# Kernel tuning notes

Hardware: AMD Instinct MI355X
Metric: run time of the kernel (lower is better)

The kernel has to match this reference:

```python
import jax, jax.numpy as jnp
import numpy as np

B = 64; WIN_IN = 32; WIN_OUT = 8; NODES = 128; FEAT = 16
HID = 64; LSTM_H = 32; CLASSES = 10
N = B * WIN_IN * NODES      # 262144 total nodes in batched graph
E = 8 * N                   # 2097152 edges (avg degree 8)


def setup_inputs() -> dict:
    key = jax.random.key(0)
    ks = jax.random.split(key, 16)
    p = lambda k, s: (jax.random.normal(k, s, dtype=jnp.float32) * 0.05)
    return {
        "x": jax.random.normal(ks[0], (N, FEAT), dtype=jnp.float32),
        "edge_index": jax.random.randint(ks[1], (2, E), 0, N, dtype=jnp.int32),
        "W1": p(ks[2], (FEAT, HID)),   "b1": p(ks[3], (HID,)),
        "W2": p(ks[4], (HID, FEAT)),   "b2": p(ks[5], (FEAT,)),
        "Wih": p(ks[6], (4 * LSTM_H, NODES * FEAT)),
        "Whh": p(ks[7], (4 * LSTM_H, LSTM_H)),
        "bih": p(ks[8], (4 * LSTM_H,)), "bhh": p(ks[9], (4 * LSTM_H,)),
        "Wfc1": p(ks[10], (16, LSTM_H)), "bfc1": p(ks[11], (16,)),
        "Wfc2": p(ks[12], (CLASSES, 16)), "bfc2": p(ks[13], (CLASSES,)),
    }


def _gcn_conv(x, row, col, W, b):
    # PyG GCNConv: x' = D^-1/2 (A+I) D^-1/2 (x W) + b, deg counted at target (col)
    h = x @ W
    deg = jax.ops.segment_sum(jnp.ones(row.shape[0], jnp.float32), col, num_segments=N) + 1.0
    dinv = jax.lax.rsqrt(deg)
    msg = h[row] * (dinv[row] * dinv[col])[:, None]          # [E, F]
    agg = jax.ops.segment_sum(msg, col, num_segments=N)
    agg = agg + h * (dinv * dinv)[:, None]                   # self-loop term
    return agg + b


def _lstm(seq, Wih, Whh, bih, bhh):
    # seq: [B, T, D] -> outputs [B, T, H]; torch gate order i, f, g, o
    xs = jnp.transpose(seq, (1, 0, 2))
    h0 = jnp.zeros((seq.shape[0], LSTM_H), seq.dtype)
    bias = bih + bhh

    def step(carry, xt):
        h, c = carry
        g = xt @ Wih.T + h @ Whh.T + bias
        i, f, gg, o = jnp.split(g, 4, axis=-1)
        c = jax.nn.sigmoid(f) * c + jax.nn.sigmoid(i) * jnp.tanh(gg)
        h = jax.nn.sigmoid(o) * jnp.tanh(c)
        return (h, c), h

    _, hs = jax.lax.scan(step, (h0, h0), xs)
    return jnp.transpose(hs, (1, 0, 2))


def reference(x, edge_index, W1, b1, W2, b2, Wih, Whh, bih, bhh, Wfc1, bfc1, Wfc2, bfc2):
    row, col = edge_index[0], edge_index[1]
    h = jax.nn.relu(_gcn_conv(x, row, col, W1, b1))
    h = jax.nn.relu(_gcn_conv(h, row, col, W2, b2))
    h = h.reshape(B, WIN_IN, NODES * FEAT)
    h = _lstm(h, Wih, Whh, bih, bhh)
    h = h[:, -WIN_OUT:, :]
    h = jax.nn.relu(h @ Wfc1.T + bfc1)
    h = h @ Wfc2.T + bfc2
    return h.reshape(-1, CLASSES)
```

## Files before the change

kernel.cpp:

```cpp
#include <hip/hip_runtime.h>
#include <hip/hip_fp16.h>

#define NN      262144
#define EDGES   2097152
#define FEATD   16
#define HIDD    64
#define LSTMH   32
#define BATCH   64
#define WIN     32
#define WOUT    8
#define NCLS    10
#define ROWD    2048
#define KCHUNKS 16
#define KSPAN   (ROWD / KCHUNKS)

#define NB2     512
#define NW      512
#define CAPB    4608
#define NBLK    256
#define CHUNK   (EDGES / NBLK)

typedef __fp16 half4v __attribute__((ext_vector_type(4)));
typedef float  float4v __attribute__((ext_vector_type(4)));

__global__ void k_hist(const int* __restrict__ ei, int* __restrict__ hist2d) {
    __shared__ int h[NB2];
    int blk = blockIdx.x, tid = threadIdx.x;
    for (int l = tid; l < NB2; l += 256) h[l] = 0;
    __syncthreads();
    int e0 = blk * CHUNK;
    for (int i = tid; i < CHUNK; i += 256)
        atomicAdd(&h[ei[EDGES + e0 + i] >> 9], 1);
    __syncthreads();
    for (int l = tid; l < NB2; l += 256) hist2d[l * NBLK + blk] = h[l];
}

__global__ void k_scan2(int* __restrict__ hist2d, int* __restrict__ bcnt) {
    __shared__ int s[NBLK];
    int b = blockIdx.x, tid = threadIdx.x;
    int v = hist2d[b * NBLK + tid];
    s[tid] = v;
    __syncthreads();
    for (int off = 1; off < NBLK; off <<= 1) {
        int t = (tid >= off) ? s[tid - off] : 0;
        __syncthreads();
        s[tid] += t;
        __syncthreads();
    }
    hist2d[b * NBLK + tid] = s[tid] - v;
    if (tid == NBLK - 1) bcnt[b] = s[tid];
}

__global__ void k_place(const int* __restrict__ ei, const int* __restrict__ hist2d,
                        int* __restrict__ bdata) {
    __shared__ int curp[NB2];
    int blk = blockIdx.x, tid = threadIdx.x;
    for (int l = tid; l < NB2; l += 256) curp[l] = hist2d[l * NBLK + blk];
    __syncthreads();
    int e0 = blk * CHUNK;
    for (int i = tid; i < CHUNK; i += 256) {
        int r = ei[e0 + i];
        int c = ei[EDGES + e0 + i];
        int b = c >> 9;
        int p = atomicAdd(&curp[b], 1);
        if (p < CAPB) bdata[(size_t)b * CAPB + p] = (r << 9) | (c & 511);
    }
}

__global__ void __launch_bounds__(512)
k_csrsort(const int* __restrict__ bcnt, const int* __restrict__ bdata,
          int* __restrict__ rows, int* __restrict__ offp, float* __restrict__ dinv,
          const float* __restrict__ x, __half2* __restrict__ xsH) {
    __shared__ int sidx[CAPB];
    __shared__ int sorted[CAPB];
    __shared__ int hist[NW], curp[NW], ssc[NW];
    __shared__ float sdinv[NW];
    int b = blockIdx.x, tid = threadIdx.x;
    int total = bcnt[b]; if (total > CAPB) total = CAPB;
    hist[tid] = 0;
    __syncthreads();
    const int* base = bdata + (size_t)b * CAPB;
    for (int i = tid; i < total; i += 512) {
        int w = base[i];
        sidx[i] = w;
        atomicAdd(&hist[w & 511], 1);
    }
    __syncthreads();
    int v = hist[tid];
    ssc[tid] = v;
    __syncthreads();
    for (int st = 1; st < NW; st <<= 1) {
        int t = (tid >= st) ? ssc[tid - st] : 0;
        __syncthreads();
        ssc[tid] += t;
        __syncthreads();
    }
    float dval = rsqrtf((float)v + 1.0f);
    curp[tid] = ssc[tid] - v;
    offp[b * NW + tid] = ssc[tid];
    dinv[b * NW + tid] = dval;
    sdinv[tid] = dval;
    __syncthreads();
    for (int i = tid; i < total; i += 512) {
        int w = sidx[i];
        int pos = atomicAdd(&curp[w & 511], 1);
        sorted[pos] = w >> 9;
    }
    for (int i = tid; i < NW * 8; i += 512) {
        int nl = i >> 3;
        float d = sdinv[nl];
        float2 xv = ((const float2*)x)[(size_t)(b * NW) * 8 + i];
        xsH[(size_t)(b * NW) * 8 + i] = __floats2half2_rn(xv.x * d, xv.y * d);
    }
    __syncthreads();
    for (int i = tid; i < total; i += 512) rows[(size_t)b * CAPB + i] = sorted[i];
}

__global__ void k_wihcvt(const float* __restrict__ Wih, __half2* __restrict__ WihH) {
    int i = blockIdx.x * blockDim.x + threadIdx.x;
    if (i >= 128 * ROWD / 4) return;
    float4 v = ((const float4*)Wih)[i];
    WihH[i * 2 + 0] = __floats2half2_rn(v.x, v.y);
    WihH[i * 2 + 1] = __floats2half2_rn(v.z, v.w);
}

template<int LAYER>
__global__ void __launch_bounds__(256)
k_aggcsr(const int* __restrict__ rows, const int* __restrict__ off,
         const float* __restrict__ dinv, const __half2* __restrict__ srcH,
         const float* __restrict__ b2, __half2* __restrict__ outH) {
    int i = blockIdx.x * blockDim.x + threadIdx.x;
    if (i >= NN * 8) return;
    int n = i >> 3, f2 = i & 7;
    int begin = (n & 511) ? off[n - 1] : 0;
    int end = off[n];
    const size_t base = (size_t)(n >> 9) * CAPB;
    float2 selfv = __half22float2(srcH[(size_t)n * 8 + f2]);
    float ax = selfv.x, ay = selfv.y;
    for (size_t e = base + begin; e < base + end; ++e) {
        int r = rows[e];
        float2 v = __half22float2(srcH[(size_t)r * 8 + f2]);
        ax += v.x; ay += v.y;
    }
    float d = dinv[n];
    ax *= d; ay *= d;
    if (LAYER == 2) {
        ax = fmaxf(ax + b2[f2 * 2 + 0], 0.f);
        ay = fmaxf(ay + b2[f2 * 2 + 1], 0.f);
    }
    outH[i] = __floats2half2_rn(ax, ay);
}

__global__ void k_gcnmlp(const __half2* __restrict__ in1H, __half2* __restrict__ xsH,
                         const float* __restrict__ dinv,
                         const float* __restrict__ W1, const float* __restrict__ b1,
                         const float* __restrict__ W2) {
    __shared__ float sW1[FEATD * HIDD];
    __shared__ float sW2[HIDD * FEATD];
    __shared__ float sb1[HIDD];
    for (int l = threadIdx.x; l < FEATD * HIDD; l += blockDim.x) {
        sW1[l] = W1[l];
        sW2[l] = W2[l];
    }
    if (threadIdx.x < HIDD) sb1[threadIdx.x] = b1[threadIdx.x];
    __syncthreads();
    int n = blockIdx.x * blockDim.x + threadIdx.x;
    if (n >= NN) return;
    union { float4 f4; __half2 h2[4]; } a0, a1;
    a0.f4 = ((const float4*)(in1H + (size_t)n * 8))[0];
    a1.f4 = ((const float4*)(in1H + (size_t)n * 8))[1];
    float in[FEATD];
#pragma unroll
    for (int q = 0; q < 4; q++) {
        float2 v = __half22float2(a0.h2[q]);
        in[q * 2 + 0] = v.x; in[q * 2 + 1] = v.y;
        v = __half22float2(a1.h2[q]);
        in[8 + q * 2 + 0] = v.x; in[8 + q * 2 + 1] = v.y;
    }
    float out[FEATD];
#pragma unroll
    for (int c = 0; c < FEATD; c++) out[c] = 0.f;
#pragma unroll 8
    for (int j = 0; j < HIDD; j++) {
        float h = sb1[j];
#pragma unroll
        for (int f = 0; f < FEATD; f++) h += in[f] * sW1[f * HIDD + j];
        h = fmaxf(h, 0.f);
#pragma unroll
        for (int c = 0; c < FEATD; c++) out[c] += h * sW2[j * FEATD + c];
    }
    float dn = dinv[n];
    union { float4 f4; __half2 h2[4]; } o0, o1;
#pragma unroll
    for (int q = 0; q < 4; q++) {
        o0.h2[q] = __floats2half2_rn(out[q * 2] * dn, out[q * 2 + 1] * dn);
        o1.h2[q] = __floats2half2_rn(out[8 + q * 2] * dn, out[8 + q * 2 + 1] * dn);
    }
    ((float4*)(xsH + (size_t)n * 8))[0] = o0.f4;
    ((float4*)(xsH + (size_t)n * 8))[1] = o1.f4;
}

__global__ void __launch_bounds__(256)
k_gemmA(const __half* __restrict__ h2, const __half* __restrict__ WihH,
        float* __restrict__ gxp) {
    __shared__ __half Bs[128][KSPAN + 8];
    int tid = threadIdx.x;
    int row0 = blockIdx.x * 32;
    int k0 = blockIdx.y * KSPAN;
    for (int idx = tid; idx < 128 * (KSPAN / 8); idx += 256) {
        int j = idx >> 4, c8 = (idx & 15) * 8;
        *(float4*)&Bs[j][c8] = *(const float4*)&WihH[(size_t)j * ROWD + k0 + c8];
    }
    __syncthreads();
    int w = tid >> 6;
    int l = tid & 63;
    int rt = w & 1;
    int ch = w >> 1;
    int m = l & 15;
    int kg = l >> 4;
    float4v acc0 = {0.f, 0.f, 0.f, 0.f};
    float4v acc1 = {0.f, 0.f, 0.f, 0.f};
    float4v acc2 = {0.f, 0.f, 0.f, 0.f};
    float4v acc3 = {0.f, 0.f, 0.f, 0.f};
    const __half* aptr = h2 + (size_t)(row0 + rt * 16 + m) * ROWD + k0 + kg * 4;
#pragma unroll
    for (int kk = 0; kk < KSPAN; kk += 16) {
        half4v a = *(const half4v*)(aptr + kk);
        half4v b0 = *(const half4v*)&Bs[ch * 64 + 0 * 16 + m][kk + kg * 4];
        half4v b1 = *(const half4v*)&Bs[ch * 64 + 1 * 16 + m][kk + kg * 4];
        half4v b2 = *(const half4v*)&Bs[ch * 64 + 2 * 16 + m][kk + kg * 4];
        half4v b3 = *(const half4v*)&Bs[ch * 64 + 3 * 16 + m][kk + kg * 4];
        acc0 = __builtin_amdgcn_mfma_f32_16x16x16f16(a, b0, acc0, 0, 0, 0);
        acc1 = __builtin_amdgcn_mfma_f32_16x16x16f16(a, b1, acc1, 0, 0, 0);
        acc2 = __builtin_amdgcn_mfma_f32_16x16x16f16(a, b2, acc2, 0, 0, 0);
        acc3 = __builtin_amdgcn_mfma_f32_16x16x16f16(a, b3, acc3, 0, 0, 0);
    }
    float* ob = gxp + (size_t)blockIdx.y * (ROWD * 128) + (size_t)(row0 + rt * 16) * 128 + ch * 64;
#pragma unroll
    for (int i = 0; i < 4; i++) {
        size_t ro = (size_t)(kg * 4 + i) * 128;
        ob[ro + 0 * 16 + m] = acc0[i];
        ob[ro + 1 * 16 + m] = acc1[i];
        ob[ro + 2 * 16 + m] = acc2[i];
        ob[ro + 3 * 16 + m] = acc3[i];
    }
}

__global__ void k_pre(const float* __restrict__ gxp, float* __restrict__ sgx) {
    int i = blockIdx.x * blockDim.x + threadIdx.x;
    if (i >= ROWD * 128) return;
    float s = 0.f;
#pragma unroll
    for (int p = 0; p < KCHUNKS; p++) s += gxp[(size_t)p * ROWD * 128 + i];
    sgx[i] = s;
}

__global__ void k_lstm(const float* __restrict__ sgx, const float* __restrict__ Whh,
                       const float* __restrict__ bih, const float* __restrict__ bhh,
                       float* __restrict__ hseq) {
    __shared__ float sWhhT[LSTMH][4 * LSTMH];
    __shared__ float sgxL[WIN * 4 * LSTMH];
    __shared__ float sh[LSTMH], sc[LSTMH], sg[4 * LSTMH];
    int b = blockIdx.x, j = threadIdx.x;
    for (int l = j; l < 4 * LSTMH * LSTMH; l += 4 * LSTMH) {
        int r = l >> 5, k = l & 31;
        sWhhT[k][r] = Whh[l];
    }
    for (int l = j; l < WIN * 128; l += 128) sgxL[l] = sgx[(size_t)b * WIN * 128 + l];
    float bias = bih[j] + bhh[j];
    if (j < LSTMH) { sh[j] = 0.f; sc[j] = 0.f; }
    __syncthreads();
    for (int t = 0; t < WIN; t++) {
        float g = bias + sgxL[t * 128 + j];
#pragma unroll
        for (int k = 0; k < LSTMH; k++) g += sWhhT[k][j] * sh[k];
        sg[j] = g;
        __syncthreads();
        if (j < LSTMH) {
            float ig = sg[j], fg = sg[32 + j], gg = sg[64 + j], og = sg[96 + j];
            float c = sc[j];
            float si = 1.f / (1.f + __expf(-ig));
            float sf = 1.f / (1.f + __expf(-fg));
            float so = 1.f / (1.f + __expf(-og));
            c = sf * c + si * tanhf(gg);
            float h = so * tanhf(c);
            sc[j] = c; sh[j] = h;
            if (t >= WIN - WOUT)
                hseq[(size_t)(b * WOUT + (t - (WIN - WOUT))) * LSTMH + j] = h;
        }
        __syncthreads();
    }
}

__global__ void k_fc(const float* __restrict__ hseq, const float* __restrict__ Wfc1,
                     const float* __restrict__ bfc1, const float* __restrict__ Wfc2,
                     const float* __restrict__ bfc2, float* __restrict__ out) {
    __shared__ float sW1[16 * 32], sb1[16], sW2[10 * 16], sb2[10];
    int tid = threadIdx.x;
    for (int l = tid; l < 16 * 32; l += blockDim.x) sW1[l] = Wfc1[l];
    if (tid < 16) sb1[tid] = bfc1[tid];
    for (int l = tid; l < 160; l += blockDim.x) sW2[l] = Wfc2[l];
    if (tid < 10) sb2[tid] = bfc2[tid];
    __syncthreads();
    int r = blockIdx.x * blockDim.x + tid;
    if (r >= BATCH * WOUT) return;
    float h[32];
#pragma unroll
    for (int k = 0; k < 32; k++) h[k] = hseq[(size_t)r * 32 + k];
    float hid[16];
#pragma unroll
    for (int j = 0; j < 16; j++) {
        float v = sb1[j];
#pragma unroll
        for (int k = 0; k < 32; k++) v += sW1[j * 32 + k] * h[k];
        hid[j] = fmaxf(v, 0.f);
    }
#pragma unroll
    for (int c = 0; c < NCLS; c++) {
        float v = sb2[c];
#pragma unroll
        for (int j = 0; j < 16; j++) v += sW2[c * 16 + j] * hid[j];
        out[(size_t)r * NCLS + c] = v;
    }
}

extern "C" void kernel_launch(void* const* d_in, const int* in_sizes, int n_in,
                              void* d_out, int out_size, void* d_ws, size_t ws_size,
                              hipStream_t stream) {
    const float* x    = (const float*)d_in[0];
    const int*   ei   = (const int*)d_in[1];
    const float* W1   = (const float*)d_in[2];
    const float* b1   = (const float*)d_in[3];
    const float* W2   = (const float*)d_in[4];
    const float* b2   = (const float*)d_in[5];
    const float* Wih  = (const float*)d_in[6];
    const float* Whh  = (const float*)d_in[7];
    const float* bih  = (const float*)d_in[8];
    const float* bhh  = (const float*)d_in[9];
    const float* Wfc1 = (const float*)d_in[10];
    const float* bfc1 = (const float*)d_in[11];
    const float* Wfc2 = (const float*)d_in[12];
    const float* bfc2 = (const float*)d_in[13];
    float* out = (float*)d_out;

    float*   ws     = (float*)d_ws;
    float*   dinv   = ws;
    int*     hist2d = (int*)(dinv + NN);
    int*     bcnt   = hist2d + NB2 * NBLK;
    int*     off    = bcnt + NB2;
    int*     rows   = off + NN;
    __half2* aggH   = (__half2*)(rows + (size_t)NB2 * CAPB);
    __half2* xsH    = aggH + (size_t)NN * 8;
    int*     bdata  = (int*)(xsH + (size_t)NN * 8);
    float*   gxp    = (float*)(bdata + (size_t)NB2 * CAPB);
    float*   sgx    = gxp + (size_t)KCHUNKS * ROWD * 128;
    float*   hseq   = sgx + ROWD * 128;
    __half2* WihH   = (__half2*)(hseq + BATCH * WOUT * LSTMH);

    k_hist<<<NBLK, 256, 0, stream>>>(ei, hist2d);
    k_scan2<<<NB2, NBLK, 0, stream>>>(hist2d, bcnt);
    k_place<<<NBLK, 256, 0, stream>>>(ei, hist2d, bdata);
    k_csrsort<<<NB2, 512, 0, stream>>>(bcnt, bdata, rows, off, dinv, x, xsH);
    k_wihcvt<<<128 * ROWD / 4 / 256, 256, 0, stream>>>(Wih, WihH);

    k_aggcsr<1><<<NN * 8 / 256, 256, 0, stream>>>(rows, off, dinv, xsH, b2, aggH);
    k_gcnmlp<<<NN / 256, 256, 0, stream>>>(aggH, xsH, dinv, W1, b1, W2);
    k_aggcsr<2><<<NN * 8 / 256, 256, 0, stream>>>(rows, off, dinv, xsH, b2, aggH);

    dim3 gg(ROWD / 32, KCHUNKS);
    k_gemmA<<<gg, 256, 0, stream>>>((const __half*)aggH, (const __half*)WihH, gxp);
    k_pre<<<ROWD * 128 / 256, 256, 0, stream>>>(gxp, sgx);
    k_lstm<<<BATCH, 128, 0, stream>>>(sgx, Whh, bih, bhh, hseq);
    k_fc<<<2, 256, 0, stream>>>(hseq, Wfc1, bfc1, Wfc2, bfc2, out);
}
```

Before: 222.3 us.

## Fuse layer-1 aggregation with GCN MLP and fold split-K reduction into LSTM

Layer-1 CSR aggregation now writes its per-node results to shared memory, and the same block then runs the W1/ReLU/W2 MLP, so the intermediate aggregate no longer goes through global memory. The split-K partial-sum kernel is removed, and the LSTM kernel sums the 16 partial GEMM outputs itself while loading its gate inputs. Buffer roles are swapped (aggH and xsH) to match. This drops two launches and one global round trip, but the LSTM runs on only 64 blocks, so the reduction now has far less parallelism. The fused kernel also uses more shared memory, which may lower occupancy.

Result: slower. 247.3 us (+11.2%).

```diff
diff --git a/kernel.cpp b/kernel.cpp
--- a/kernel.cpp
+++ b/kernel.cpp
@@ -124,11 +124,73 @@
     WihH[i * 2 + 1] = __floats2half2_rn(v.z, v.w);
 }
 
-template<int LAYER>
 __global__ void __launch_bounds__(256)
-k_aggcsr(const int* __restrict__ rows, const int* __restrict__ off,
-         const float* __restrict__ dinv, const __half2* __restrict__ srcH,
-         const float* __restrict__ b2, __half2* __restrict__ outH) {
+k_agg1mlp(const int* __restrict__ rows, const int* __restrict__ off,
+          const float* __restrict__ dinv, const __half2* __restrict__ xsH,
+          const float* __restrict__ W1, const float* __restrict__ b1,
+          const float* __restrict__ W2, __half2* __restrict__ t2sH) {
+    __shared__ float sin[256][FEATD + 1];
+    __shared__ float sW1[FEATD * HIDD];
+    __shared__ float sW2[HIDD * FEATD];
+    __shared__ float sb1[HIDD];
+    int tid = threadIdx.x;
+    for (int l = tid; l < FEATD * HIDD; l += 256) {
+        sW1[l] = W1[l];
+        sW2[l] = W2[l];
+    }
+    if (tid < HIDD) sb1[tid] = b1[tid];
+    int nbase = blockIdx.x * 256;
+    int f2 = tid & 7;
+    int nl = tid >> 3;
+#pragma unroll
+    for (int s = 0; s < 8; s++) {
+        int n = nbase + s * 32 + nl;
+        int begin = (n & 511) ? off[n - 1] : 0;
+        int end = off[n];
+        const size_t base = (size_t)(n >> 9) * CAPB;
+        float2 sv = __half22float2(xsH[(size_t)n * 8 + f2]);
+        float ax = sv.x, ay = sv.y;
+        for (size_t e = base + begin; e < base + end; ++e) {
+            int r = rows[e];
+            float2 v = __half22float2(xsH[(size_t)r * 8 + f2]);
+            ax += v.x; ay += v.y;
+        }
+        float d = dinv[n];
+        sin[s * 32 + nl][f2 * 2 + 0] = ax * d;
+        sin[s * 32 + nl][f2 * 2 + 1] = ay * d;
+    }
+    __syncthreads();
+    int n = nbase + tid;
+    float in[FEATD];
+#pragma unroll
+    for (int f = 0; f < FEATD; f++) in[f] = sin[tid][f];
+    float out[FEATD];
+#pragma unroll
+    for (int c = 0; c < FEATD; c++) out[c] = 0.f;
+#pragma unroll 8
+    for (int j = 0; j < HIDD; j++) {
+        float h = sb1[j];
+#pragma unroll
+        for (int f = 0; f < FEATD; f++) h += in[f] * sW1[f * HIDD + j];
+        h = fmaxf(h, 0.f);
+#pragma unroll
+        for (int c = 0; c < FEATD; c++) out[c] += h * sW2[j * FEATD + c];
+    }
+    float dn = dinv[n];
+    union { float4 f4; __half2 h2[4]; } o0, o1;
+#pragma unroll
+    for (int q = 0; q < 4; q++) {
+        o0.h2[q] = __floats2half2_rn(out[q * 2] * dn, out[q * 2 + 1] * dn);
+        o1.h2[q] = __floats2half2_rn(out[8 + q * 2] * dn, out[8 + q * 2 + 1] * dn);
+    }
+    ((float4*)(t2sH + (size_t)n * 8))[0] = o0.f4;
+    ((float4*)(t2sH + (size_t)n * 8))[1] = o1.f4;
+}
+
+__global__ void __launch_bounds__(256)
+k_aggcsr2(const int* __restrict__ rows, const int* __restrict__ off,
+          const float* __restrict__ dinv, const __half2* __restrict__ srcH,
+          const float* __restrict__ b2, __half2* __restrict__ outH) {
     int i = blockIdx.x * blockDim.x + threadIdx.x;
     if (i >= NN * 8) return;
     int n = i >> 3, f2 = i & 7;
@@ -143,61 +205,9 @@
         ax += v.x; ay += v.y;
     }
     float d = dinv[n];
-    ax *= d; ay *= d;
-    if (LAYER == 2) {
-        ax = fmaxf(ax + b2[f2 * 2 + 0], 0.f);
-        ay = fmaxf(ay + b2[f2 * 2 + 1], 0.f);
-    }
+    ax = fmaxf(ax * d + b2[f2 * 2 + 0], 0.f);
+    ay = fmaxf(ay * d + b2[f2 * 2 + 1], 0.f);
     outH[i] = __floats2half2_rn(ax, ay);
-}
-
-__global__ void k_gcnmlp(const __half2* __restrict__ in1H, __half2* __restrict__ xsH,
-                         const float* __restrict__ dinv,
-                         const float* __restrict__ W1, const float* __restrict__ b1,
-                         const float* __restrict__ W2) {
-    __shared__ float sW1[FEATD * HIDD];
-    __shared__ float sW2[HIDD * FEATD];
-    __shared__ float sb1[HIDD];
-    for (int l = threadIdx.x; l < FEATD * HIDD; l += blockDim.x) {
-        sW1[l] = W1[l];
-        sW2[l] = W2[l];
-    }
-    if (threadIdx.x < HIDD) sb1[threadIdx.x] = b1[threadIdx.x];
-    __syncthreads();
-    int n = blockIdx.x * blockDim.x + threadIdx.x;
-    if (n >= NN) return;
-    union { float4 f4; __half2 h2[4]; } a0, a1;
-    a0.f4 = ((const float4*)(in1H + (size_t)n * 8))[0];
-    a1.f4 = ((const float4*)(in1H + (size_t)n * 8))[1];
-    float in[FEATD];
-#pragma unroll
-    for (int q = 0; q < 4; q++) {
-        float2 v = __half22float2(a0.h2[q]);
-        in[q * 2 + 0] = v.x; in[q * 2 + 1] = v.y;
-        v = __half22float2(a1.h2[q]);
-        in[8 + q * 2 + 0] = v.x; in[8 + q * 2 + 1] = v.y;
-    }
-    float out[FEATD];
-#pragma unroll
-    for (int c = 0; c < FEATD; c++) out[c] = 0.f;
-#pragma unroll 8
-    for (int j = 0; j < HIDD; j++) {
-        float h = sb1[j];
-#pragma unroll
-        for (int f = 0; f < FEATD; f++) h += in[f] * sW1[f * HIDD + j];
-        h = fmaxf(h, 0.f);
-#pragma unroll
-        for (int c = 0; c < FEATD; c++) out[c] += h * sW2[j * FEATD + c];
-    }
-    float dn = dinv[n];
-    union { float4 f4; __half2 h2[4]; } o0, o1;
-#pragma unroll
-    for (int q = 0; q < 4; q++) {
-        o0.h2[q] = __floats2half2_rn(out[q * 2] * dn, out[q * 2 + 1] * dn);
-        o1.h2[q] = __floats2half2_rn(out[8 + q * 2] * dn, out[8 + q * 2 + 1] * dn);
-    }
-    ((float4*)(xsH + (size_t)n * 8))[0] = o0.f4;
-    ((float4*)(xsH + (size_t)n * 8))[1] = o1.f4;
 }
 
 __global__ void __launch_bounds__(256)
@@ -246,16 +256,7 @@
     }
 }
 
-__global__ void k_pre(const float* __restrict__ gxp, float* __restrict__ sgx) {
-    int i = blockIdx.x * blockDim.x + threadIdx.x;
-    if (i >= ROWD * 128) return;
-    float s = 0.f;
-#pragma unroll
-    for (int p = 0; p < KCHUNKS; p++) s += gxp[(size_t)p * ROWD * 128 + i];
-    sgx[i] = s;
-}
-
-__global__ void k_lstm(const float* __restrict__ sgx, const float* __restrict__ Whh,
+__global__ void k_lstm(const float* __restrict__ gxp, const float* __restrict__ Whh,
                        const float* __restrict__ bih, const float* __restrict__ bhh,
                        float* __restrict__ hseq) {
     __shared__ float sWhhT[LSTMH][4 * LSTMH];
@@ -266,7 +267,13 @@
         int r = l >> 5, k = l & 31;
         sWhhT[k][r] = Whh[l];
     }
-    for (int l = j; l < WIN * 128; l += 128) sgxL[l] = sgx[(size_t)b * WIN * 128 + l];
+    for (int l = j; l < WIN * 128; l += 128) {
+        float s = 0.f;
+#pragma unroll
+        for (int p = 0; p < KCHUNKS; p++)
+            s += gxp[(size_t)p * ROWD * 128 + (size_t)b * WIN * 128 + l];
+        sgxL[l] = s;
+    }
     float bias = bih[j] + bhh[j];
     if (j < LSTMH) { sh[j] = 0.f; sc[j] = 0.f; }
     __syncthreads();
@@ -353,8 +360,7 @@
     __half2* xsH    = aggH + (size_t)NN * 8;
     int*     bdata  = (int*)(xsH + (size_t)NN * 8);
     float*   gxp    = (float*)(bdata + (size_t)NB2 * CAPB);
-    float*   sgx    = gxp + (size_t)KCHUNKS * ROWD * 128;
-    float*   hseq   = sgx + ROWD * 128;
+    float*   hseq   = gxp + (size_t)KCHUNKS * ROWD * 128;
     __half2* WihH   = (__half2*)(hseq + BATCH * WOUT * LSTMH);
 
     k_hist<<<NBLK, 256, 0, stream>>>(ei, hist2d);
@@ -363,13 +369,11 @@
     k_csrsort<<<NB2, 512, 0, stream>>>(bcnt, bdata, rows, off, dinv, x, xsH);
     k_wihcvt<<<128 * ROWD / 4 / 256, 256, 0, stream>>>(Wih, WihH);
 
-    k_aggcsr<1><<<NN * 8 / 256, 256, 0, stream>>>(rows, off, dinv, xsH, b2, aggH);
-    k_gcnmlp<<<NN / 256, 256, 0, stream>>>(aggH, xsH, dinv, W1, b1, W2);
-    k_aggcsr<2><<<NN * 8 / 256, 256, 0, stream>>>(rows, off, dinv, xsH, b2, aggH);
+    k_agg1mlp<<<NN / 256, 256, 0, stream>>>(rows, off, dinv, xsH, W1, b1, W2, aggH);
+    k_aggcsr2<<<NN * 8 / 256, 256, 0, stream>>>(rows, off, dinv, aggH, b2, xsH);
 
     dim3 gg(ROWD / 32, KCHUNKS);
-    k_gemmA<<<gg, 256, 0, stream>>>((const __half*)aggH, (const __half*)WihH, gxp);
-    k_pre<<<ROWD * 128 / 256, 256, 0, stream>>>(gxp, sgx);
-    k_lstm<<<BATCH, 128, 0, stream>>>(sgx, Whh, bih, bhh, hseq);
+    k_gemmA<<<gg, 256, 0, stream>>>((const __half*)xsH, (const __half*)WihH, gxp);
+    k_lstm<<<BATCH, 128, 0, stream>>>(gxp, Whh, bih, bhh, hseq);
     k_fc<<<2, 256, 0, stream>>>(hseq, Wfc1, bfc1, Wfc2, bfc2, out);
 }
```
